# Performance work log

Measured on AMD Instinct MI355X. Metric: run time of the kernel, lower is better.

Reference implementation:

```python
import jax, jax.numpy as jnp
import numpy as np

B, N, D = 8, 1024, 256   # batch, nodes, input_size
H, HO = 4, 64            # nhead, hidden_size/nhead
T = 5                    # number of edge types (len(edges))
NEG = -1e9
EPS = 1e-6


def setup_inputs() -> dict:
    key = jax.random.key(0)
    ks = jax.random.split(key, 6)
    nodes_embed = jax.random.normal(ks[0], (B, N, D), dtype=jnp.float32)
    node_adj = jax.random.randint(ks[1], (B, N, N), 0, T + 1)  # values 0..T, 0 = no edge
    # per-head projection W: xavier-ish scale
    W = jax.random.normal(ks[2], (H, D, HO), dtype=jnp.float32) * (1.0 / np.sqrt(D))
    # per-edge-type scoring linear (2*HO -> 1), split into src/dst halves
    a_src = jax.random.normal(ks[3], (H, T, HO), dtype=jnp.float32) * 0.1
    a_dst = jax.random.normal(ks[4], (H, T, HO), dtype=jnp.float32) * 0.1
    bias = jnp.zeros((H, HO), dtype=jnp.float32)
    ln_gamma = jnp.ones((H, HO), dtype=jnp.float32)
    ln_beta = jnp.zeros((H, HO), dtype=jnp.float32)
    return {
        'nodes_embed': nodes_embed,
        'node_adj': node_adj,
        'W': W,
        'a_src': a_src,
        'a_dst': a_dst,
        'bias': bias,
        'ln_gamma': ln_gamma,
        'ln_beta': ln_beta,
    }


def reference(nodes_embed, node_adj, W, a_src, a_dst, bias, ln_gamma, ln_beta):
    # h: [B, H, N, HO] -- all heads projected at once
    h = jnp.einsum('bnd,hde->bhne', nodes_embed, W)
    # The torch code concatenates [h_i, h_j] and applies a (2*HO -> 1) linear per
    # edge type; that equals e_src[t, i] + e_dst[t, j] with the linear weight split
    # into src/dst halves. Avoids materializing the O(N^2 * 2*HO) concat tensor.
    e_src = jnp.einsum('bhne,hte->bhtn', h, a_src)  # [B, H, T, N]
    e_dst = jnp.einsum('bhne,hte->bhtn', h, a_dst)  # [B, H, T, N]
    n_types = a_src.shape[1]
    weight = jnp.zeros(h.shape[:2] + (h.shape[2], h.shape[2]), dtype=h.dtype)  # [B,H,N,N]
    for t in range(n_types):  # small fixed loop over edge types
        mask = (node_adj == t + 1).astype(h.dtype)[:, None]  # [B,1,N,N]
        weight = weight + mask * (e_src[:, :, t, :, None] + e_dst[:, :, t, None, :])
    weight = jax.nn.leaky_relu(weight, negative_slope=0.01)
    weight = jnp.where(node_adj[:, None] == 0, NEG, weight)
    attention = jax.nn.softmax(weight, axis=-1)  # [B,H,N,N]
    dst = jnp.einsum('bhij,bhje->bhie', attention, h) + bias[None, :, None, :]
    out = jax.nn.relu(dst) + h  # dropout is identity (p=0)
    # per-head LayerNorm over HO, eps=1e-6 (biased variance, as torch)
    mu = out.mean(axis=-1, keepdims=True)
    var = out.var(axis=-1, keepdims=True)
    out = (out - mu) / jnp.sqrt(var + EPS) * ln_gamma[None, :, None, :] + ln_beta[None, :, None, :]
    # concat heads: [B,H,N,HO] -> [B,N,H*HO]
    b, hh, n, e = out.shape
    return out.transpose(0, 2, 1, 3).reshape(b, n, hh * e)
```

## Files before the change

kernel.cpp:

```cpp
#include <hip/hip_runtime.h>
#include <hip/hip_bf16.h>

#define Bn 8
#define Nn 1024
#define Dn 256
#define Hn 4
#define HOn 64
#define Tn 5
#define WTR 80
#define EDS 128

typedef short bf16x8 __attribute__((ext_vector_type(8)));
typedef float f32x4 __attribute__((ext_vector_type(4)));

__device__ __forceinline__ float b2f(unsigned short u) {
    unsigned x = ((unsigned)u) << 16;
    float f;
    __builtin_memcpy(&f, &x, 4);
    return f;
}
__device__ __forceinline__ unsigned bfr(float f) {
    unsigned u;
    __builtin_memcpy(&u, &f, 4);
    return (u + 0x7FFFu + ((u >> 16) & 1u)) >> 16;
}
__device__ __forceinline__ unsigned short f2b(float f) { return (unsigned short)bfr(f); }

__device__ __forceinline__ float fast_exp2(float x) {
#if __has_builtin(__builtin_amdgcn_exp2f)
    return __builtin_amdgcn_exp2f(x);
#else
    float r;
    asm("v_exp_f32 %0, %1" : "=v"(r) : "v"(x));
    return r;
#endif
}

__global__ __launch_bounds__(256) void k_signal(float* __restrict__ out, int n) {
    int i = blockIdx.x * 256 + threadIdx.x;
    if (i < n) out[i] = 100.0f;
}

__global__ __launch_bounds__(256) void k_transpose_w(const float* __restrict__ W,
                                                     const float* __restrict__ a_src,
                                                     const float* __restrict__ a_dst,
                                                     unsigned short* __restrict__ WT) {
    __shared__ float tile[64][65];
    int h = blockIdx.x >> 2;
    int d0 = (blockIdx.x & 3) * 64;
    int c0 = threadIdx.x & 63;
    int r0 = threadIdx.x >> 6;
#pragma unroll
    for (int r = 0; r < 16; r++) {
        int d = r * 4 + r0;
        tile[d][c0] = W[((size_t)(h * Dn + d0 + d)) * HOn + c0];
    }
    __syncthreads();
#pragma unroll
    for (int r = 0; r < 16; r++) {
        int e = r * 4 + r0;
        WT[((size_t)(h * WTR + e)) * Dn + d0 + c0] = f2b(tile[c0][e]);
    }
    for (int t = r0; t < 2 * Tn; t += 4) {
        const float* av = (t < Tn) ? (a_src + (h * Tn + t) * HOn)
                                   : (a_dst + (h * Tn + t - Tn) * HOn);
        float s = 0.f;
#pragma unroll
        for (int e = 0; e < HOn; e++) s += tile[c0][e] * av[e];
        WT[((size_t)(h * WTR + 64 + t)) * Dn + d0 + c0] = f2b(s);
    }
    for (int rr = 74 + r0; rr < WTR; rr += 4)
        WT[((size_t)(h * WTR + rr)) * Dn + d0 + c0] = 0;
}

__global__ __launch_bounds__(256) void k_proj(const float* __restrict__ X,
                                              const unsigned short* __restrict__ WT,
                                              const int* __restrict__ adj,
                                              unsigned short* __restrict__ hP,
                                              float* __restrict__ e_src,
                                              float* __restrict__ e_dst,
                                              unsigned* __restrict__ adjp) {
    __shared__ unsigned short ptile[4][64][24];
    int tid = threadIdx.x;
    int w = tid >> 6;
    int lane = tid & 63;
    int quad = lane >> 4;
    int l15 = lane & 15;
    int b = blockIdx.x >> 6;
    int i0 = (blockIdx.x & 63) * 16;
    int h = w;
    int bh = b * Hn + h;

    {
        const int* arow = adj + ((size_t)(b * Nn + i0)) * Nn;
        unsigned* aout = adjp + ((size_t)(b * Nn + i0)) * Nn / 4;
#pragma unroll 4
        for (int k = 0; k < 16; k++) {
            int idx = tid + k * 256;
            int4 v = *(const int4*)(arow + (size_t)idx * 4);
            unsigned pk = (unsigned)(v.x & 0xFF) | ((unsigned)(v.y & 0xFF) << 8) |
                          ((unsigned)(v.z & 0xFF) << 16) | ((unsigned)(v.w & 0xFF) << 24);
            aout[idx] = pk;
        }
    }

    bf16x8 Bx[8];
    const float* xf = X + ((size_t)(b * Nn + i0 + l15)) * Dn + quad * 8;
#pragma unroll
    for (int kc = 0; kc < 8; kc++) {
        union { bf16x8 v; unsigned u[4]; } uu;
        const float4* xp = (const float4*)(xf + kc * 32);
        float4 A0 = xp[0], A1 = xp[1];
        __hip_bfloat162 h0 = __float22bfloat162_rn(make_float2(A0.x, A0.y));
        __hip_bfloat162 h1 = __float22bfloat162_rn(make_float2(A0.z, A0.w));
        __hip_bfloat162 h2 = __float22bfloat162_rn(make_float2(A1.x, A1.y));
        __hip_bfloat162 h3 = __float22bfloat162_rn(make_float2(A1.z, A1.w));
        __builtin_memcpy(&uu.u[0], &h0, 4);
        __builtin_memcpy(&uu.u[1], &h1, 4);
        __builtin_memcpy(&uu.u[2], &h2, 4);
        __builtin_memcpy(&uu.u[3], &h3, 4);
        Bx[kc] = uu.v;
    }

    f32x4 acc[5] = {{0.f, 0.f, 0.f, 0.f}, {0.f, 0.f, 0.f, 0.f}, {0.f, 0.f, 0.f, 0.f},
                    {0.f, 0.f, 0.f, 0.f}, {0.f, 0.f, 0.f, 0.f}};
    const unsigned short* wbase = WT + (size_t)h * WTR * Dn;
#pragma unroll
    for (int kc = 0; kc < 8; kc++) {
#pragma unroll
        for (int et = 0; et < 5; et++) {
            bf16x8 Aw = *(const bf16x8*)(wbase + (size_t)(et * 16 + l15) * Dn + kc * 32 + quad * 8);
            acc[et] = __builtin_amdgcn_mfma_f32_16x16x32_bf16(Aw, Bx[kc], acc[et], 0, 0, 0);
        }
    }

#pragma unroll
    for (int et = 0; et < 4; et++) {
#pragma unroll
        for (int reg = 0; reg < 4; reg++) {
            int e = et * 16 + quad * 4 + reg;
            ptile[w][e][l15] = f2b(acc[et][reg]);
        }
    }
    {
        int jb = i0 >> 4;
        int e_lo = lane >> 5;
        int l15v = (lane >> 1) & 15;
        int q2 = lane & 1;
#pragma unroll
        for (int p = 0; p < 2; p++) {
            int et = 2 * p + e_lo;
            bf16x8 v = *(const bf16x8*)(&ptile[w][et * 16 + l15v][q2 * 8]);
            *(bf16x8*)(hP + (((size_t)bh * 64 + jb) * 4 + et) * 256 + l15v * 16 + q2 * 8) = v;
        }
    }
#pragma unroll
    for (int reg = 0; reg < 4; reg++) {
        int t = quad * 4 + reg;
        if (t < Tn)
            e_src[((size_t)bh * Tn + t) * Nn + i0 + l15] = acc[4][reg] * 1.4426950408889634f;
        else if (t < 2 * Tn)
            e_dst[((size_t)bh * Tn + (t - Tn)) * Nn + i0 + l15] = acc[4][reg] * 1.4426950408889634f;
    }
}

__global__ __launch_bounds__(512) void k_attn(const unsigned char* __restrict__ adjp,
                                              const float* __restrict__ e_src,
                                              const float* __restrict__ e_dst,
                                              const unsigned short* __restrict__ hP,
                                              const float* __restrict__ bias,
                                              const float* __restrict__ gamma,
                                              const float* __restrict__ beta,
                                              float* __restrict__ out) {
    __shared__ __align__(16) unsigned short p_lds[8][16][136];
    __shared__ float es2[4][16][8];
    __shared__ float l_lds[8][16];
    __shared__ __align__(16) float ed_lds[8][6 * EDS];
    float* macc = (float*)&p_lds[4][0][0];

    int tid = threadIdx.x;
    int w = tid >> 6;
    int lane = tid & 63;
    int quad = lane >> 4;
    int l15 = lane & 15;
    int hh = w & 3;
    int half = w >> 2;
    int b = blockIdx.x >> 6;
    int i0 = (blockIdx.x & 63) * 16;
    int bh = b * Hn + hh;
    int J0 = half * 512;

    const unsigned char* adj_base = adjp + ((size_t)(b * Nn + i0)) * Nn + J0;
    const float* edst = e_dst + (size_t)bh * Tn * Nn + J0;
    const unsigned short* hPb = hP + (size_t)bh * 64 * 1024;

    int c0 = 2 * lane;
    float* edw = &ed_lds[w][0];

    f32x4 acc[4] = {{0.f, 0.f, 0.f, 0.f}, {0.f, 0.f, 0.f, 0.f},
                    {0.f, 0.f, 0.f, 0.f}, {0.f, 0.f, 0.f, 0.f}};
    f32x4 accl = {0.f, 0.f, 0.f, 0.f};
    bf16x8 ONES;
    {
        short o = (short)0x3F80;
        ONES = (bf16x8){o, o, o, o, o, o, o, o};
    }

    edw[c0] = -3e38f;
    edw[c0 + 1] = -3e38f;

    unsigned adjC[16], adjN[16];
#pragma unroll
    for (int r = 0; r < 16; r++)
        adjC[r] = *(const unsigned short*)(adj_base + (size_t)r * Nn + c0);
    float2 edr[Tn];
#pragma unroll
    for (int t = 0; t < Tn; t++) edr[t] = *(const float2*)(edst + t * Nn + c0);

    if (w < 4) {
        const float* esrc = e_src + (size_t)bh * Tn * Nn;
#pragma unroll
        for (int idx = lane; idx < 96; idx += 64) {
            int t = idx >> 4, row = idx & 15;
            es2[w][row][t] = t ? esrc[(t - 1) * Nn + i0 + row] : 0.f;
        }
    }
    __syncthreads();

#define P1ROW(ROW, AV)                                                          \
    {                                                                           \
        int a0 = (int)((AV) & 0xFFu);                                           \
        int a1 = (int)((AV) >> 8);                                              \
        float e0 = es2[hh][ROW][a0];                                            \
        float e1 = es2[hh][ROW][a1];                                            \
        float d0 = edw[a0 * EDS + c0];                                          \
        float d1 = edw[a1 * EDS + c0 + 1];                                      \
        float x0 = e0 + d0; x0 = fmaxf(x0, 0.01f * x0);                         \
        float x1 = e1 + d1; x1 = fmaxf(x1, 0.01f * x1);                         \
        float p0 = fast_exp2(x0);                                               \
        float p1 = fast_exp2(x1);                                               \
        __hip_bfloat162 pp = __float22bfloat162_rn(make_float2(p0, p1));        \
        unsigned pu; __builtin_memcpy(&pu, &pp, 4);                             \
        *(unsigned*)(&p_lds[w][ROW][2 * lane]) = pu;                            \
    }

#pragma unroll 1
    for (int c = 0; c < 4; c++) {
        int jc = c * 128;
#pragma unroll
        for (int t = 0; t < Tn; t++) {
            int wi = (t + 1) * EDS + c0;
            edw[wi] = edr[t].x;
            edw[wi + 1] = edr[t].y;
        }
        if (c < 3) {
#pragma unroll
            for (int r = 0; r < 16; r++)
                adjN[r] = *(const unsigned short*)(adj_base + (size_t)r * Nn + jc + 128 + c0);
#pragma unroll
            for (int t = 0; t < Tn; t++)
                edr[t] = *(const float2*)(edst + t * Nn + jc + 128 + c0);
        }
#pragma unroll
        for (int r = 0; r < 16; r++) P1ROW(r, adjC[r]);
#pragma unroll
        for (int k = 0; k < 4; k++) {
            bf16x8 Afr = *(const bf16x8*)(&p_lds[w][l15][k * 32 + quad * 8]);
            accl = __builtin_amdgcn_mfma_f32_16x16x32_bf16(Afr, ONES, accl, 0, 0, 0);
            int jb = ((J0 + jc + k * 32) >> 4) + (quad >> 1);
#pragma unroll
            for (int et = 0; et < 4; et++) {
                bf16x8 Bf = *(const bf16x8*)(hPb + ((size_t)jb * 4 + et) * 256 +
                                             l15 * 16 + (quad & 1) * 8);
                acc[et] = __builtin_amdgcn_mfma_f32_16x16x32_bf16(Afr, Bf, acc[et], 0, 0, 0);
            }
        }
        if (c < 3) {
#pragma unroll
            for (int r = 0; r < 16; r++) adjC[r] = adjN[r];
        }
    }
#undef P1ROW

    if (l15 == 0) {
#pragma unroll
        for (int reg = 0; reg < 4; reg++) l_lds[w][quad * 4 + reg] = accl[reg];
    }
    __syncthreads();
    if (w >= 4) {
#pragma unroll
        for (int et = 0; et < 4; et++)
#pragma unroll
            for (int reg = 0; reg < 4; reg++)
                macc[((hh * 16) + quad * 4 + reg) * 64 + et * 16 + l15] = acc[et][reg];
    }
    __syncthreads();
    if (w >= 4) return;

    float bv[4], gv[4], bev[4];
#pragma unroll
    for (int et = 0; et < 4; et++) {
        int e = et * 16 + l15;
        bv[et] = bias[hh * HOn + e];
        gv[et] = gamma[hh * HOn + e];
        bev[et] = beta[hh * HOn + e];
    }
    int jbe = i0 >> 4;
#pragma unroll
    for (int reg = 0; reg < 4; reg++) {
        int r = quad * 4 + reg;
        int i = i0 + r;
        float lw = l_lds[w][r] + l_lds[w + 4][r];
        float linv = 1.f / fmaxf(lw, 1e-30f);
        float dv[4];
        float s = 0.f, ss = 0.f;
        int q2 = r >> 3, m = r & 7;
#pragma unroll
        for (int et = 0; et < 4; et++) {
            int e = et * 16 + l15;
            float v = (acc[et][reg] + macc[((hh * 16) + r) * 64 + e]) * linv + bv[et];
            v = (v > 0.f) ? v : 0.f;
            v += b2f(hPb[((size_t)jbe * 4 + et) * 256 + l15 * 16 + q2 * 8 + m]);
            dv[et] = v;
            s += v;
            ss += v * v;
        }
#pragma unroll
        for (int off = 8; off; off >>= 1) {
            s += __shfl_xor(s, off);
            ss += __shfl_xor(ss, off);
        }
        float mean = s * (1.f / 64.f);
        float var = ss * (1.f / 64.f) - mean * mean;
        float rstd = rsqrtf(var + 1e-6f);
#pragma unroll
        for (int et = 0; et < 4; et++) {
            int e = et * 16 + l15;
            float o = (dv[et] - mean) * rstd * gv[et] + bev[et];
            out[((size_t)(b * Nn + i)) * (Hn * HOn) + hh * HOn + e] = o;
        }
    }
}

extern "C" void kernel_launch(void* const* d_in, const int* in_sizes, int n_in,
                              void* d_out, int out_size, void* d_ws, size_t ws_size,
                              hipStream_t stream) {
    const float* X = (const float*)d_in[0];
    const int* adj = (const int*)d_in[1];
    const float* W = (const float*)d_in[2];
    const float* a_src = (const float*)d_in[3];
    const float* a_dst = (const float*)d_in[4];
    const float* bias = (const float*)d_in[5];
    const float* gamma = (const float*)d_in[6];
    const float* beta = (const float*)d_in[7];
    float* out = (float*)d_out;

    char* ws = (char*)d_ws;
    size_t off = 0;
    unsigned short* hP = (unsigned short*)(ws + off);  off += (size_t)Bn * Hn * Nn * HOn * 2;
    unsigned short* WT = (unsigned short*)(ws + off);  off += (size_t)Hn * WTR * Dn * 2;
    float* e_src = (float*)(ws + off);                 off += (size_t)Bn * Hn * Tn * Nn * 4;
    float* e_dst = (float*)(ws + off);                 off += (size_t)Bn * Hn * Tn * Nn * 4;
    unsigned char* adjp = (unsigned char*)(ws + off);  off += (size_t)Bn * Nn * Nn;

    if (ws_size < off) {
        k_signal<<<(out_size + 255) / 256, 256, 0, stream>>>(out, out_size);
        return;
    }

    k_transpose_w<<<Hn * (Dn / 64), 256, 0, stream>>>(W, a_src, a_dst, WT);
    k_proj<<<Bn * (Nn / 16), 256, 0, stream>>>(X, WT, adj, hP, e_src, e_dst, (unsigned*)adjp);
    k_attn<<<Bn * (Nn / 16), 512, 0, stream>>>(adjp, e_src, e_dst, hP, bias, gamma, beta, out);
}
```

Baseline: 132.1 us.

## Pre-pack projection weights in MFMA fragment order and stage X via LDS

The weight-prep kernel now writes W (plus the folded a_src/a_dst rows) in an MFMA-fragment-packed layout, so each lane in k_proj loads its A operand with contiguous coalesced 16-byte reads instead of strided row reads. k_proj also loads its 16x256 X tile cooperatively with coalesced float4 loads, converts it to bf16 into shared memory, and then reads B fragments from LDS. This trades the scattered global access pattern for an extra barrier and shared-memory traffic. It also adds a full waitcnt before the ptile readback.

After: 124.0 us (median of 2 runs). 6.1% less time.

```diff
diff --git a/kernel.cpp b/kernel.cpp
--- a/kernel.cpp
+++ b/kernel.cpp
@@ -44,8 +44,9 @@
 __global__ __launch_bounds__(256) void k_transpose_w(const float* __restrict__ W,
                                                      const float* __restrict__ a_src,
                                                      const float* __restrict__ a_dst,
-                                                     unsigned short* __restrict__ WT) {
+                                                     unsigned short* __restrict__ WP) {
     __shared__ float tile[64][65];
+    __shared__ float arow_s[10][64];
     int h = blockIdx.x >> 2;
     int d0 = (blockIdx.x & 3) * 64;
     int c0 = threadIdx.x & 63;
@@ -56,30 +57,47 @@
         tile[d][c0] = W[((size_t)(h * Dn + d0 + d)) * HOn + c0];
     }
     __syncthreads();
-#pragma unroll
-    for (int r = 0; r < 16; r++) {
-        int e = r * 4 + r0;
-        WT[((size_t)(h * WTR + e)) * Dn + d0 + c0] = f2b(tile[c0][e]);
-    }
     for (int t = r0; t < 2 * Tn; t += 4) {
         const float* av = (t < Tn) ? (a_src + (h * Tn + t) * HOn)
                                    : (a_dst + (h * Tn + t - Tn) * HOn);
         float s = 0.f;
 #pragma unroll
         for (int e = 0; e < HOn; e++) s += tile[c0][e] * av[e];
-        WT[((size_t)(h * WTR + 64 + t)) * Dn + d0 + c0] = f2b(s);
-    }
-    for (int rr = 74 + r0; rr < WTR; rr += 4)
-        WT[((size_t)(h * WTR + rr)) * Dn + d0 + c0] = 0;
+        arow_s[t][c0] = s;
+    }
+    __syncthreads();
+    int kcb = d0 >> 5;
+#pragma unroll
+    for (int it = 0; it < 3; it++) {
+        int idx = threadIdx.x + it * 256;
+        if (idx < 640) {
+            int kcp = idx / 320;
+            int rem = idx % 320;
+            int et = rem >> 6;
+            int ln = rem & 63;
+            int quad = ln >> 4, l15 = ln & 15;
+            int dl = kcp * 32 + quad * 8;
+            int row = et * 16 + l15;
+            union { bf16x8 v; unsigned short u[8]; } ov;
+#pragma unroll
+            for (int m = 0; m < 8; m++) {
+                float x = (row < 64) ? tile[dl + m][row]
+                                     : ((row < 74) ? arow_s[row - 64][dl + m] : 0.f);
+                ov.u[m] = f2b(x);
+            }
+            *(bf16x8*)(WP + ((((size_t)h * 8 + kcb + kcp) * 5 + et) * 64 + ln) * 8) = ov.v;
+        }
+    }
 }
 
 __global__ __launch_bounds__(256) void k_proj(const float* __restrict__ X,
-                                              const unsigned short* __restrict__ WT,
+                                              const unsigned short* __restrict__ WP,
                                               const int* __restrict__ adj,
                                               unsigned short* __restrict__ hP,
                                               float* __restrict__ e_src,
                                               float* __restrict__ e_dst,
                                               unsigned* __restrict__ adjp) {
+    __shared__ unsigned short xs[16][264];
     __shared__ unsigned short ptile[4][64][24];
     int tid = threadIdx.x;
     int w = tid >> 6;
@@ -104,32 +122,35 @@
         }
     }
 
+#pragma unroll
+    for (int it = 0; it < 4; it++) {
+        int row = it * 4 + (tid >> 6);
+        int col = (tid & 63) * 4;
+        float4 v = *(const float4*)(X + ((size_t)(b * Nn + i0 + row)) * Dn + col);
+        __hip_bfloat162 h0 = __float22bfloat162_rn(make_float2(v.x, v.y));
+        __hip_bfloat162 h1 = __float22bfloat162_rn(make_float2(v.z, v.w));
+        unsigned u0, u1;
+        __builtin_memcpy(&u0, &h0, 4);
+        __builtin_memcpy(&u1, &h1, 4);
+        unsigned* dst = (unsigned*)&xs[row][col];
+        dst[0] = u0;
+        dst[1] = u1;
+    }
+    __syncthreads();
+
     bf16x8 Bx[8];
-    const float* xf = X + ((size_t)(b * Nn + i0 + l15)) * Dn + quad * 8;
-#pragma unroll
-    for (int kc = 0; kc < 8; kc++) {
-        union { bf16x8 v; unsigned u[4]; } uu;
-        const float4* xp = (const float4*)(xf + kc * 32);
-        float4 A0 = xp[0], A1 = xp[1];
-        __hip_bfloat162 h0 = __float22bfloat162_rn(make_float2(A0.x, A0.y));
-        __hip_bfloat162 h1 = __float22bfloat162_rn(make_float2(A0.z, A0.w));
-        __hip_bfloat162 h2 = __float22bfloat162_rn(make_float2(A1.x, A1.y));
-        __hip_bfloat162 h3 = __float22bfloat162_rn(make_float2(A1.z, A1.w));
-        __builtin_memcpy(&uu.u[0], &h0, 4);
-        __builtin_memcpy(&uu.u[1], &h1, 4);
-        __builtin_memcpy(&uu.u[2], &h2, 4);
-        __builtin_memcpy(&uu.u[3], &h3, 4);
-        Bx[kc] = uu.v;
-    }
+#pragma unroll
+    for (int kc = 0; kc < 8; kc++)
+        Bx[kc] = *(const bf16x8*)(&xs[l15][kc * 32 + quad * 8]);
 
     f32x4 acc[5] = {{0.f, 0.f, 0.f, 0.f}, {0.f, 0.f, 0.f, 0.f}, {0.f, 0.f, 0.f, 0.f},
                     {0.f, 0.f, 0.f, 0.f}, {0.f, 0.f, 0.f, 0.f}};
-    const unsigned short* wbase = WT + (size_t)h * WTR * Dn;
+    const unsigned short* wbase = WP + (size_t)h * 8 * 5 * 64 * 8;
 #pragma unroll
     for (int kc = 0; kc < 8; kc++) {
 #pragma unroll
         for (int et = 0; et < 5; et++) {
-            bf16x8 Aw = *(const bf16x8*)(wbase + (size_t)(et * 16 + l15) * Dn + kc * 32 + quad * 8);
+            bf16x8 Aw = *(const bf16x8*)(wbase + (((size_t)kc * 5 + et) * 64 + lane) * 8);
             acc[et] = __builtin_amdgcn_mfma_f32_16x16x32_bf16(Aw, Bx[kc], acc[et], 0, 0, 0);
         }
     }
@@ -142,6 +163,7 @@
             ptile[w][e][l15] = f2b(acc[et][reg]);
         }
     }
+    __builtin_amdgcn_s_waitcnt(0);
     {
         int jb = i0 >> 4;
         int e_lo = lane >> 5;
@@ -358,7 +380,7 @@
     char* ws = (char*)d_ws;
     size_t off = 0;
     unsigned short* hP = (unsigned short*)(ws + off);  off += (size_t)Bn * Hn * Nn * HOn * 2;
-    unsigned short* WT = (unsigned short*)(ws + off);  off += (size_t)Hn * WTR * Dn * 2;
+    unsigned short* WP = (unsigned short*)(ws + off);  off += (size_t)Hn * WTR * Dn * 2;
     float* e_src = (float*)(ws + off);                 off += (size_t)Bn * Hn * Tn * Nn * 4;
     float* e_dst = (float*)(ws + off);                 off += (size_t)Bn * Hn * Tn * Nn * 4;
     unsigned char* adjp = (unsigned char*)(ws + off);  off += (size_t)Bn * Nn * Nn;
@@ -368,7 +390,7 @@
         return;
     }
 
-    k_transpose_w<<<Hn * (Dn / 64), 256, 0, stream>>>(W, a_src, a_dst, WT);
-    k_proj<<<Bn * (Nn / 16), 256, 0, stream>>>(X, WT, adj, hP, e_src, e_dst, (unsigned*)adjp);
+    k_transpose_w<<<Hn * (Dn / 64), 256, 0, stream>>>(W, a_src, a_dst, WP);
+    k_proj<<<Bn * (Nn / 16), 256, 0, stream>>>(X, WP, adj, hP, e_src, e_dst, (unsigned*)adjp);
     k_attn<<<Bn * (Nn / 16), 512, 0, stream>>>(adjp, e_src, e_dst, hP, bias, gamma, beta, out);
 }
```
